# Kernel tuning notes

Hardware: AMD Instinct MI355X
Metric: run time of the kernel (lower is better)

## Reference

```python
import jax, jax.numpy as jnp
import numpy as np
from jax.scipy.special import i0

# NUFFT adjoint (gridding) configuration, matching m_op.plan(uv, (256,256), (512,512), (6,6))
N = 256          # image side
K = 512
J = 6            # kernel support per dim
B = 8            # batch
M = 100000       # n_measurements
ALPHA = K / N    # oversampling = 2
BETA = float(np.pi * np.sqrt((J / ALPHA * (ALPHA - 0.5)) ** 2 - 0.8))  # Fessler KB beta


def setup_inputs() -> dict:
    key = jax.random.key(0)
    k1, k2, k3, k4 = jax.random.split(key, 4)
    y_real = jax.random.normal(k1, (B, M), dtype=jnp.float32)
    y_imag = jax.random.normal(k2, (B, M), dtype=jnp.float32)
    weights = jax.random.uniform(k3, (M,), dtype=jnp.float32, minval=0.1, maxval=1.0)
    uv = jax.random.uniform(k4, (M, 2), dtype=jnp.float32,
                            minval=-np.pi, maxval=np.pi)
    return {"y_real": y_real, "y_imag": y_imag, "weights": weights, "uv": uv}


def _kb(t):
    # Kaiser-Bessel interpolation kernel, support |t| <= J/2
    u = 2.0 * t / J
    return i0(BETA * jnp.sqrt(jnp.clip(1.0 - u * u, 0.0))) / i0(jnp.asarray(BETA, jnp.float32))


def reference(y_real, y_imag, weights, uv):
    # weighted complex measurements: inputs * measurement_weights
    y = (y_real + 1j * y_imag) * weights[None, :]           # (B, M) complex64

    # map uv in [-pi, pi) to oversampled grid coords in [0, K)
    kf = uv * (K / (2.0 * np.pi))                            # (M, 2), DC at index 0 (mod K)
    base = jnp.floor(kf).astype(jnp.int32)                   # (M, 2)
    offs = jnp.arange(-J // 2 + 1, J // 2 + 1)               # [-2..3], 6 taps
    idx = base[:, :, None] + offs[None, None, :]             # (M, 2, J)
    dist = idx.astype(jnp.float32) - kf[:, :, None]
    w = _kb(dist)                                            # (M, 2, J) separable weights
    idxm = jnp.mod(idx, K)                                   # wrap onto torus

    w2 = (w[:, 0, :, None] * w[:, 1, None, :]).reshape(M, J * J)          # (M, 36)
    lin = (idxm[:, 0, :, None] * K + idxm[:, 1, None, :]).reshape(M * J * J)
    vals = (y[:, :, None] * w2[None, :, :].astype(jnp.complex64)).reshape(B, M * J * J)

    # scatter-add onto oversampled Fourier grid
    grid = jnp.zeros((B, K * K), jnp.complex64).at[:, lin].add(vals)
    grid = grid.reshape(B, K, K)

    # inverse FFT, center, crop to N x N
    img = jnp.fft.fftshift(jnp.fft.ifft2(grid), axes=(1, 2))
    c = K // 2
    img = img[:, c - N // 2:c + N // 2, c - N // 2:c + N // 2]

    # deapodization: divide by 1D FT of the KB kernel (always real here since BETA > pi*J/4*... )
    n = jnp.arange(N, dtype=jnp.float32) - N // 2
    xf = np.pi * J * n / K
    arg = BETA * BETA - xf * xf
    d = jnp.sinh(jnp.sqrt(arg)) / jnp.sqrt(arg)              # (N,)
    apod = d[:, None] * d[None, :]

    x = (jnp.real(img) / apod).astype(jnp.float32)           # tf.math.real(adj_op(...))

    # per-image min-max rescale
    tmax = jnp.max(x, axis=(1, 2), keepdims=True)
    tmin = jnp.min(x, axis=(1, 2), keepdims=True)
    return (x - tmin) / (tmax - tmin)
```

## Files before the change

### kernel.cpp

```cpp
#include <hip/hip_runtime.h>
#include <math.h>

#define NN 256
#define KK 512
#define JJ 6
#define BB 8
#define MPTS 100000
#define NBINS (KK * KK)
#define KF_SCALE 81.48733086305615f

typedef _Float16 h8 __attribute__((ext_vector_type(8)));
typedef _Float16 h2 __attribute__((ext_vector_type(2)));


__device__ __forceinline__ float i0f_dev(float x) {
    float ax = fabsf(x);
    if (ax < 3.75f) {
        float t = x / 3.75f; t *= t;
        return 1.0f + t*(3.5156229f + t*(3.0899424f + t*(1.2067492f +
               t*(0.2659732f + t*(0.0360768f + t*0.0045813f)))));
    } else {
        float t = 3.75f / ax;
        return (expf(ax) * rsqrtf(ax)) *
               (0.39894228f + t*(0.01328592f + t*(0.00225319f + t*(-0.00157565f +
                t*(0.00916281f + t*(-0.02057706f + t*(0.02635537f +
                t*(-0.01647633f + t*0.00392377f))))))));
    }
}

__device__ __forceinline__ float kbf(float t, float beta, float inv_i0b) {
    float u = t * (1.0f / 3.0f);
    float q = fmaxf(1.0f - u * u, 0.0f);
    return i0f_dev(beta * sqrtf(q)) * inv_i0b;
}

__device__ __forceinline__ int wave_scan(int x, int lane) {
#pragma unroll
    for (int off = 1; off < 64; off <<= 1) {
        int y = __shfl_up(x, off, 64);
        if (lane >= off) x += y;
    }
    return x;
}

__device__ __forceinline__ void build_row_prefix(const int* __restrict__ btot,
                                                 int* sPref, int t)
{
    if (t < 64) {
        int carry = 0;
        if (t == 0) sPref[0] = 0;
#pragma unroll
        for (int k = 0; k < 8; ++k) {
            int x = btot[k * 64 + t];
            int incl = wave_scan(x, t);
            sPref[k * 64 + t + 1] = incl + carry;
            carry += __shfl(incl, 63, 64);
        }
    }
}

__device__ __forceinline__ float kb_lut(const float* __restrict__ sT, float t) {
    float u = (t + 3.0f) * (1023.0f / 6.0f);
    int i = (int)u;
    i = min(i, 1022);
    float f = u - (float)i;
    float a = sT[i];
    return a + f * (sT[i + 1] - sT[i]);
}

__device__ __forceinline__ void tw_lookup(const float* __restrict__ twc,
                                          const float* __restrict__ tws,
                                          int idx, float& wr, float& wi) {
    float sg = (idx & 256) ? -1.0f : 1.0f;
    int ib = idx & 255;
    wr = sg * twc[ib];
    wi = sg * tws[ib];
}


__device__ __forceinline__ void fill_point(
    const float2* __restrict__ uv2,
    const float* __restrict__ y_real, const float* __restrict__ y_imag,
    const float* __restrict__ weights, const int* __restrict__ offsets,
    const int* sPref,
    int* counts, char* rec, const float* sT, int m)
{
    float2 u = uv2[m];
    float kf0 = u.x * KF_SCALE;
    float kf1 = u.y * KF_SCALE;
    float f0 = floorf(kf0), f1 = floorf(kf1);
    float fr0 = kf0 - f0, fr1 = kf1 - f1;
    int b0r = (int)f0 & (KK - 1);
    int b1c = (int)f1 & (KK - 1);
    int bin = (b0r << 9) | b1c;
    int old = atomicSub(&counts[bin], 1);
    int slot = sPref[b0r] + offsets[bin] + old - 1;

    _Float16 hw[12];
#pragma unroll
    for (int j = 0; j < JJ; ++j) {
        hw[j]     = (_Float16)kb_lut(sT, (float)(j - 2) - fr0);
        hw[6 + j] = (_Float16)kb_lut(sT, (float)(j - 2) - fr1);
    }

    float4 c0v, c1v;
    _Float16* p0 = (_Float16*)&c0v;
    _Float16* p1 = (_Float16*)&c1v;
#pragma unroll
    for (int j = 0; j < 8; ++j) p0[j] = hw[j];
#pragma unroll
    for (int j = 0; j < 4; ++j) p1[j] = hw[8 + j];
    ((int*)&c1v)[2] = b1c;
    ((int*)&c1v)[3] = 0;

    float wm = weights[m];
    h8 ha, hb;
#pragma unroll
    for (int b = 0; b < 4; ++b) {
        ha[2 * b]     = (_Float16)(y_real[b * MPTS + m] * wm);
        ha[2 * b + 1] = (_Float16)(y_imag[b * MPTS + m] * wm);
        hb[2 * b]     = (_Float16)(y_real[(b + 4) * MPTS + m] * wm);
        hb[2 * b + 1] = (_Float16)(y_imag[(b + 4) * MPTS + m] * wm);
    }

    float4* dst = (float4*)(rec + (size_t)slot * 64);
    dst[0] = c0v;
    dst[1] = c1v;
    dst[2] = *(float4*)&ha;
    dst[3] = *(float4*)&hb;
}

__device__ __forceinline__ void gather_strip(
    const int* __restrict__ offsets, const int* sPref,
    const char* __restrict__ rec,
    h2* __restrict__ gridh, char* myl, int j, int w, int lane)
{
    int half = lane >> 5;
    int l32 = lane & 31;
    int xcd = j & 7;
    int c0 = (xcd << 6) + ((j >> 3) & 63);
    int q4 = j >> 9;
    int c1base = (q4 << 7) + (w << 5);
    int c1 = c1base + l32;
    int wa = c1 - 3, wb = c1 + 2;

    float aR[4], aI[4];
#pragma unroll
    for (int b = 0; b < 4; ++b) { aR[b] = 0.0f; aI[b] = 0.0f; }

    for (int j0 = 0; j0 < JJ; ++j0) {
        int r0 = (c0 - (j0 - 2)) & (KK - 1);
        int rowbase = r0 << 9;
        int P = sPref[r0];
        int lo = c1base - 3, hi = c1base + 33;
        int nseg, ga0, gb0, ga1, gb1;
        if (lo < 0)        { ga0 = lo; gb0 = -1;  ga1 = 0;   gb1 = hi; nseg = 2; }
        else if (hi > 511) { ga0 = lo; gb0 = 511; ga1 = 512; gb1 = hi; nseg = 2; }
        else               { ga0 = lo; gb0 = hi;  ga1 = 0;   gb1 = 0;  nseg = 1; }

        for (int sgi = 0; sgi < nseg; ++sgi) {
            int ga = sgi ? ga1 : ga0;
            int gb = sgi ? gb1 : gb0;
            int pstart = P + offsets[rowbase + (ga & 511)];
            int ce = (gb & 511) + 1;
            int pend = (ce == 512) ? sPref[r0 + 1]
                                   : P + offsets[rowbase + ce];
            int ia = max(wa, ga), ib = min(wb, gb);
            bool has = ia <= ib;
            int pA = has ? P + offsets[rowbase + (ia & 511)] : 0;
            int pB = has ? ((ib == gb) ? pend
                                       : P + offsets[rowbase + ((ib + 1) & 511)]) : 0;

            for (int pc = pstart; pc < pend; pc += 32) {
                int cnt = min(32, pend - pc);
                int sub = lane & 3;
                int prow = lane >> 2;
#pragma unroll
                for (int qq = 0; qq < 2; ++qq) {
                    if (16 * qq < cnt) {
                        int pp = min(pc + prow + 16 * qq, MPTS - 1);
                        float4 v = *(const float4*)(rec + (size_t)pp * 64 + sub * 16);
                        *(float4*)(myl + (prow + 16 * qq) * 88 + sub * 16) = v;
                    }
                }
                int pLo = max(pA, pc), pHi = min(pB, pc + cnt);
                for (int p = pLo; p < pHi; ++p) {
                    const char* rp = myl + (p - pc) * 88;
                    int bin1 = *(const int*)(rp + 24);
                    int idx = (c1 - bin1 + 2) & 511;
                    bool ok = idx <= 5;
                    idx = ok ? idx : 0;
                    float w0 = (float)*(const _Float16*)(rp + j0 * 2);
                    float w1 = (float)*(const _Float16*)(rp + 12 + idx * 2);
                    float ww = ok ? w0 * w1 : 0.0f;
                    h8 yv = *(const h8*)(rp + 32 + (half << 4));
#pragma unroll
                    for (int b = 0; b < 4; ++b) {
                        aR[b] += (float)yv[2 * b]     * ww;
                        aI[b] += (float)yv[2 * b + 1] * ww;
                    }
                }
            }
        }
    }

    int c = (c0 << 9) + c1;
#pragma unroll
    for (int b = 0; b < 4; ++b) {
        h2 v;
        v[0] = (_Float16)aR[b];
        v[1] = (_Float16)aI[b];
        gridh[((size_t)((half << 2) + b) << 18) + c] = v;
    }
}

__device__ __forceinline__ void wave_fft512(float xr[8], float xi[8], int lane,
                                            const float* __restrict__ twc,
                                            const float* __restrict__ tws)
{
    float a0r = xr[0]+xr[4], a0i = xi[0]+xi[4];
    float a4r = xr[0]-xr[4], a4i = xi[0]-xi[4];
    float a2r = xr[2]+xr[6], a2i = xi[2]+xi[6];
    float a6r = xr[2]-xr[6], a6i = xi[2]-xi[6];
    float a1r = xr[1]+xr[5], a1i = xi[1]+xi[5];
    float a5r = xr[1]-xr[5], a5i = xi[1]-xi[5];
    float a3r = xr[3]+xr[7], a3i = xi[3]+xi[7];
    float a7r = xr[3]-xr[7], a7i = xi[3]-xi[7];
    float b0r = a0r+a2r, b0i = a0i+a2i;
    float b2r = a0r-a2r, b2i = a0i-a2i;
    float b4r = a4r-a6i, b4i = a4i+a6r;
    float b6r = a4r+a6i, b6i = a4i-a6r;
    float b1r = a1r+a3r, b1i = a1i+a3i;
    float b3r = a1r-a3r, b3i = a1i-a3i;
    float b5r = a5r-a7i, b5i = a5i+a7r;
    float b7r = a5r+a7i, b7i = a5i-a7r;
    const float S2 = 0.70710678118654752f;
    float w5r = S2*(b5r-b5i), w5i = S2*(b5r+b5i);
    float w7r = -S2*(b7r+b7i), w7i = S2*(b7r-b7i);
    float y1r = b4r+w5r, y1i = b4i+w5i;
    float y5r = b4r-w5r, y5i = b4i-w5i;
    float y2r = b2r-b3i, y2i = b2i+b3r;
    float y6r = b2r+b3i, y6i = b2i-b3r;
    float y3r = b6r+w7r, y3i = b6i+w7i;
    float y7r = b6r-w7r, y7i = b6i-w7i;

    int p = __brev((unsigned)lane) >> 26;
    xr[0] = b0r+b1r; xi[0] = b0i+b1i;
    {
        float wr, wi;
        tw_lookup(twc, tws, p,     wr, wi); xr[1] = y1r*wr - y1i*wi; xi[1] = y1i*wr + y1r*wi;
        tw_lookup(twc, tws, p * 2, wr, wi); xr[2] = y2r*wr - y2i*wi; xi[2] = y2i*wr + y2r*wi;
        tw_lookup(twc, tws, p * 3, wr, wi); xr[3] = y3r*wr - y3i*wi; xi[3] = y3i*wr + y3r*wi;
        float y4r = b0r-b1r, y4i = b0i-b1i;
        tw_lookup(twc, tws, p * 4, wr, wi); xr[4] = y4r*wr - y4i*wi; xi[4] = y4i*wr + y4r*wi;
        tw_lookup(twc, tws, p * 5, wr, wi); xr[5] = y5r*wr - y5i*wi; xi[5] = y5i*wr + y5r*wi;
        tw_lookup(twc, tws, p * 6, wr, wi); xr[6] = y6r*wr - y6i*wi; xi[6] = y6i*wr + y6r*wi;
        tw_lookup(twc, tws, p * 7, wr, wi); xr[7] = y7r*wr - y7i*wi; xi[7] = y7i*wr + y7r*wi;
    }

#pragma unroll
    for (int t = 0; t < 6; ++t) {
        int m = 1 << t;
        int j = lane & (m - 1);
        int ti = j << (8 - t);
        float wc = twc[ti], wsn = tws[ti];
        bool hi = (lane & m) != 0;
#pragma unroll
        for (int d = 0; d < 8; ++d) {
            float pR = __shfl_xor(xr[d], m, 64);
            float pI = __shfl_xor(xi[d], m, 64);
            float bR = hi ? xr[d] : pR;
            float bI = hi ? xi[d] : pI;
            float aR = hi ? pR : xr[d];
            float aI = hi ? pI : xi[d];
            float wbR = wc * bR - wsn * bI;
            float wbI = wc * bI + wsn * bR;
            xr[d] = hi ? aR - wbR : aR + wbR;
            xi[d] = hi ? aI - wbI : aI + wbI;
        }
    }
}

__device__ __forceinline__ void wave_fft256(float xr[4], float xi[4], int lane,
                                            const float* __restrict__ twc,
                                            const float* __restrict__ tws)
{
    float t0r = xr[0]+xr[2], t0i = xi[0]+xi[2];
    float t1r = xr[0]-xr[2], t1i = xi[0]-xi[2];
    float t2r = xr[1]+xr[3], t2i = xi[1]+xi[3];
    float t3r = xr[1]-xr[3], t3i = xi[1]-xi[3];
    float y1r = t1r-t3i, y1i = t1i+t3r;
    float y3r = t1r+t3i, y3i = t1i-t3r;

    int p2 = (__brev((unsigned)lane) >> 26) << 1;
    xr[0] = t0r+t2r; xi[0] = t0i+t2i;
    {
        float wr, wi;
        tw_lookup(twc, tws, p2,     wr, wi); xr[1] = y1r*wr - y1i*wi; xi[1] = y1i*wr + y1r*wi;
        float y2r = t0r-t2r, y2i = t0i-t2i;
        tw_lookup(twc, tws, p2 * 2, wr, wi); xr[2] = y2r*wr - y2i*wi; xi[2] = y2i*wr + y2r*wi;
        tw_lookup(twc, tws, p2 * 3, wr, wi); xr[3] = y3r*wr - y3i*wi; xi[3] = y3i*wr + y3r*wi;
    }

#pragma unroll
    for (int t = 0; t < 6; ++t) {
        int m = 1 << t;
        int j = lane & (m - 1);
        int ti = j << (8 - t);
        float wc = twc[ti], wsn = tws[ti];
        bool hi = (lane & m) != 0;
#pragma unroll
        for (int d = 0; d < 4; ++d) {
            float pR = __shfl_xor(xr[d], m, 64);
            float pI = __shfl_xor(xi[d], m, 64);
            float bR = hi ? xr[d] : pR;
            float bI = hi ? xi[d] : pI;
            float aR = hi ? pR : xr[d];
            float aI = hi ? pI : xi[d];
            float wbR = wc * bR - wsn * bI;
            float wbI = wc * bI + wsn * bR;
            xr[d] = hi ? aR - wbR : aR + wbR;
            xi[d] = hi ? aI - wbI : aI + wbI;
        }
    }
}

__device__ __forceinline__ void fftA_body(const h2* __restrict__ gridh,
                                          h2* __restrict__ Ch, int bx, int t,
                                          float* sR, float* sI,
                                          float* twc, float* tws)
{
    int lane = t & 63;
    int w = t >> 6;
    int x  = bx & 7;
    int b  = (bx >> 3) & 7;
    int k1base = (x << 6) | (((bx >> 6) & 7) << 3);
    int k1 = k1base + w;

    if (t < 256) {
        float ang = (float)(2.0 * M_PI / 512.0) * (float)t;
        float s, c; sincosf(ang, &s, &c);
        twc[t] = c; tws[t] = s;
    }

    const h2* row = gridh + ((size_t)b << 18) + ((size_t)k1 << 9);
    int p = __brev((unsigned)lane) >> 26;
    float xr[8], xi[8];
#pragma unroll
    for (int a = 0; a < 8; ++a) {
        h2 v = row[p + (a << 6)];
        xr[a] = (float)v[0]; xi[a] = (float)v[1];
    }
    __syncthreads();

    wave_fft512(xr, xi, lane, twc, tws);

    bool act = (lane < 16) | (lane >= 48);
    int lpp = (lane < 16) ? lane : (lane - 32);
    if (act) {
#pragma unroll
        for (int d = 0; d < 8; ++d) {
            int addr = w * 264 + d * 33 + lpp;
            sR[addr] = xr[d];
            sI[addr] = xi[d];
        }
    }
    __syncthreads();

#pragma unroll
    for (int pp = 0; pp < 4; ++pp) {
        int idx = pp * 512 + t;
        int kk = idx & 7;
        int s2 = idx >> 3;
        int v = (s2 + 128) & 255;
        int d = v & 7;
        int lp = v >> 3;
        int addr = kk * 264 + d * 33 + lp;
        h2 o;
        o[0] = (_Float16)sR[addr];
        o[1] = (_Float16)sI[addr];
        Ch[(((size_t)(b << 8) + s2) << 9) + k1base + kk] = o;
    }
}

__device__ __forceinline__ void fftB_body(const h2* __restrict__ Ch,
                                          float* __restrict__ imgT, float beta2,
                                          float* __restrict__ pmin,
                                          float* __restrict__ pmax,
                                          int bx, int t,
                                          float* twc, float* tws, float* invd,
                                          float (*wor)[256], float* wmn, float* wmx)
{
    int lane = t & 63;
    int w = t >> 6;
    int row = w >> 1;
    int odd = w & 1;
    int rowid = bx * 4 + row;
    int b = rowid >> 8;
    int s2 = rowid & 255;

    if (t < 256) {
        float ang = (float)(2.0 * M_PI / 512.0) * (float)t;
        float s, c; sincosf(ang, &s, &c);
        twc[t] = c; tws[t] = s;
    } else if (t < 512) {
        int i = t - 256;
        const float XF = (float)(M_PI * (double)JJ / (double)KK);
        float n = (float)(i - 128);
        float xf = XF * n;
        float arg = beta2 - xf * xf;
        float sq = sqrtf(arg);
        invd[i] = sq / sinhf(sq);
    }

    const h2* rowp = Ch + ((size_t)rowid << 9);
    int p = __brev((unsigned)lane) >> 26;
    float xr[4], xi[4];
#pragma unroll
    for (int a = 0; a < 4; ++a) {
        h2 v = rowp[((p + (a << 6)) << 1) | odd];
        xr[a] = (float)v[0]; xi[a] = (float)v[1];
    }
    __syncthreads();

    wave_fft256(xr, xi, lane, twc, tws);

    if (odd) {
        float4 wo;
#pragma unroll
        for (int d = 0; d < 4; ++d) {
            int k = (lane << 2) + d;
            ((float*)&wo)[d] = xr[d] * twc[k] - xi[d] * tws[k];
        }
        *(float4*)&wor[row][lane << 2] = wo;
    }
    __syncthreads();

    if (!odd) {
        const float INVK2 = 1.0f / ((float)KK * (float)KK);
        float sbase = INVK2 * invd[s2];
        float lmin = 1e30f, lmax = -1e30f;
        float4 wo = *(const float4*)&wor[row][lane << 2];
        float vals[4];
#pragma unroll
        for (int d = 0; d < 4; ++d) {
            int k = (lane << 2) + d;
            float e = xr[d];
            float woK = ((const float*)&wo)[d];
            float xre = (k < 128) ? (e + woK) : (e - woK);
            int r = (k + 128) & 255;
            float o = xre * sbase * invd[r];
            vals[d] = o;
            lmin = fminf(lmin, o);
            lmax = fmaxf(lmax, o);
        }
        int r0run = ((lane << 2) + 128) & 255;
        *(float4*)(imgT + ((size_t)b << 16) + (s2 << 8) + r0run) =
            make_float4(vals[0], vals[1], vals[2], vals[3]);
#pragma unroll
        for (int off = 32; off >= 1; off >>= 1) {
            lmin = fminf(lmin, __shfl_xor(lmin, off, 64));
            lmax = fmaxf(lmax, __shfl_xor(lmax, off, 64));
        }
        if (lane == 0) { wmn[row] = lmin; wmx[row] = lmax; }
    }
    __syncthreads();
    if (t == 0) {
        float mn = fminf(fminf(wmn[0], wmn[1]), fminf(wmn[2], wmn[3]));
        float mx = fmaxf(fmaxf(wmx[0], wmx[1]), fmaxf(wmx[2], wmx[3]));
        pmin[bx] = mn;
        pmax[bx] = mx;
    }
}

__device__ __forceinline__ void norm_body(const float* __restrict__ imgT,
                                          const float* __restrict__ pmin,
                                          const float* __restrict__ pmax,
                                          float* __restrict__ out,
                                          int bx, int t, int nthr,
                                          float (*tile)[65], float* s_mn, float* s_inv)
{
    int b = bx >> 4;
    int tl = bx & 15;
    int r0 = (tl & 3) << 6;
    int s0 = (tl >> 2) << 6;
    int tr = t & 63;
    int ts = t >> 6;
    int nts = nthr >> 6;

    if (t < 64) {
        float mn = pmin[(b << 6) + t];
        float mx = pmax[(b << 6) + t];
#pragma unroll
        for (int off = 32; off >= 1; off >>= 1) {
            mn = fminf(mn, __shfl_xor(mn, off, 64));
            mx = fmaxf(mx, __shfl_xor(mx, off, 64));
        }
        if (t == 0) { *s_mn = mn; *s_inv = 1.0f / (mx - mn); }
    }

    const float* src = imgT + ((size_t)b << 16);
    for (int s2i = ts; s2i < 64; s2i += nts)
        tile[s2i][tr] = src[((s0 + s2i) << 8) + r0 + tr];
    __syncthreads();

    float mn = *s_mn, inv = *s_inv;
    float* dst = out + ((size_t)b << 16);
    for (int ri = ts; ri < 64; ri += nts)
        dst[((r0 + ri) << 8) + s0 + tr] = (tile[tr][ri] - mn) * inv;
}


__global__ __launch_bounds__(256) void count_bins(
    const float2* __restrict__ uv2, int* __restrict__ counts,
    float* __restrict__ lut, float beta, float inv_i0b)
{
    int m = blockIdx.x * 256 + threadIdx.x;
    if (m < 1024) {
        float t = -3.0f + (6.0f / 1023.0f) * (float)m;
        lut[m] = kbf(t, beta, inv_i0b);
    }
    if (m >= MPTS) return;
    float2 u = uv2[m];
    int b0 = (int)floorf(u.x * KF_SCALE) & (KK - 1);
    int b1 = (int)floorf(u.y * KF_SCALE) & (KK - 1);
    atomicAdd(&counts[(b0 << 9) | b1], 1);
}

__global__ __launch_bounds__(512) void scan_a(
    const int* __restrict__ counts, int* __restrict__ offsets,
    int* __restrict__ btot)
{
    __shared__ int part[8];
    int t = threadIdx.x;
    int lane = t & 63;
    int w8 = t >> 6;
    int gid = blockIdx.x * 512 + t;

    int v = counts[gid];
    int x = wave_scan(v, lane);
    if (lane == 63) part[w8] = x;
    __syncthreads();
    if (t < 8) {
        int pq = part[t];
#pragma unroll
        for (int off = 1; off < 8; off <<= 1) {
            int y = __shfl_up(pq, off, 64);
            if (t >= off) pq += y;
        }
        part[t] = pq;
    }
    __syncthreads();
    int incl = x + ((w8 > 0) ? part[w8 - 1] : 0);
    offsets[gid] = incl - v;
    if (t == 511) btot[blockIdx.x] = incl;
}

__global__ __launch_bounds__(256) void fill_records(
    const float2* __restrict__ uv2,
    const float* __restrict__ y_real, const float* __restrict__ y_imag,
    const float* __restrict__ weights, const int* __restrict__ offsets,
    const int* __restrict__ btot,
    int* __restrict__ counts, char* __restrict__ rec,
    const float* __restrict__ lut)
{
    __shared__ float sT[1024];
    __shared__ int sPref[513];
    int tid = threadIdx.x;
#pragma unroll
    for (int q = 0; q < 4; ++q) sT[q * 256 + tid] = lut[q * 256 + tid];
    build_row_prefix(btot, sPref, tid);
    __syncthreads();
    int m = blockIdx.x * 256 + tid;
    if (m >= MPTS) return;
    fill_point(uv2, y_real, y_imag, weights, offsets, sPref, counts, rec, sT, m);
}

__global__ __launch_bounds__(256) void gather_grid(
    const int* __restrict__ offsets, const int* __restrict__ btot,
    const char* __restrict__ rec, h2* __restrict__ gridh)
{
    __shared__ __align__(16) char lds[4][2816];
    __shared__ int sPref[513];
    int t = threadIdx.x;
    build_row_prefix(btot, sPref, t);
    __syncthreads();
    gather_strip(offsets, sPref, rec, gridh, lds[t >> 6], blockIdx.x,
                 t >> 6, t & 63);
}

__global__ __launch_bounds__(512) void fftA(
    const h2* __restrict__ gridh, h2* __restrict__ Ch)
{
    __shared__ float sR[2112], sI[2112];
    __shared__ float twc[256], tws[256];
    fftA_body(gridh, Ch, blockIdx.x, threadIdx.x, sR, sI, twc, tws);
}

__global__ __launch_bounds__(512) void fftB(
    const h2* __restrict__ Ch, float* __restrict__ imgT, float beta2,
    float* __restrict__ pmin, float* __restrict__ pmax)
{
    __shared__ float twc[256], tws[256];
    __shared__ float invd[256];
    __shared__ __align__(16) float wor[4][256];
    __shared__ float wmn[4], wmx[4];
    fftB_body(Ch, imgT, beta2, pmin, pmax, blockIdx.x, threadIdx.x,
              twc, tws, invd, wor, wmn, wmx);
}

__global__ __launch_bounds__(256) void norm_t(
    const float* __restrict__ imgT, const float* __restrict__ pmin,
    const float* __restrict__ pmax, float* __restrict__ out)
{
    __shared__ float tile[64][65];
    __shared__ float s_mn, s_inv;
    norm_body(imgT, pmin, pmax, out, blockIdx.x, threadIdx.x, 256,
              tile, &s_mn, &s_inv);
}


static double i0_host(double x) {
    double sum = 1.0, term = 1.0;
    double q = x * x * 0.25;
    for (int k = 1; k < 80; ++k) {
        term *= q / ((double)k * (double)k);
        sum += term;
        if (term < sum * 1e-17) break;
    }
    return sum;
}

extern "C" void kernel_launch(void* const* d_in, const int* in_sizes, int n_in,
                              void* d_out, int out_size, void* d_ws, size_t ws_size,
                              hipStream_t stream)
{
    const float* y_real  = (const float*)d_in[0];
    const float* y_imag  = (const float*)d_in[1];
    const float* weights = (const float*)d_in[2];
    const float2* uv2    = (const float2*)d_in[3];
    float* out = (float*)d_out;

    char* W = (char*)d_ws;
    h2*       gridh   = (h2*)W;
    int*      counts  = (int*)W;
    float*    imgT    = (float*)W;
    char*     A       = W + (size_t)16 * 1024 * 1024;
    char*     rec     = A;
    int*      offsets = (int*)(A + 6400000);
    h2*       Ch      = (h2*)A;
    float*    pmin    = (float*)(A + 8400000);
    float*    pmax    = (float*)(A + 8402048);
    float*    lut     = (float*)(A + 8404096);
    int*      btot    = (int*)(A + 8408192);

    double beta_d = M_PI * sqrt(19.45);
    float beta = (float)beta_d;
    float inv_i0b = (float)(1.0 / i0_host(beta_d));
    float beta2 = (float)(beta_d * beta_d);

    hipMemsetAsync(counts, 0, NBINS * sizeof(int), stream);

    count_bins<<<(MPTS + 255) / 256, 256, 0, stream>>>(
        uv2, counts, lut, beta, inv_i0b);

    scan_a<<<512, 512, 0, stream>>>(counts, offsets, btot);

    fill_records<<<(MPTS + 255) / 256, 256, 0, stream>>>(
        uv2, y_real, y_imag, weights, offsets, btot, counts, rec, lut);

    gather_grid<<<2048, 256, 0, stream>>>(offsets, btot, rec, gridh);

    fftA<<<512, 512, 0, stream>>>(gridh, Ch);

    fftB<<<512, 512, 0, stream>>>(Ch, imgT, beta2, pmin, pmax);

    norm_t<<<128, 256, 0, stream>>>(imgT, pmin, pmax, out);
}
```

Before: 139.2 us.

## Gather per-lane bin ranges directly from global records, dropping the LDS staging

The gather kernel used to stage each strip's point records into LDS cooperatively in chunks of 32, and every lane scanned the whole window while masking out bins it did not own. Now each lane loads the bin offsets once, shares them across the wave with shuffles, and walks only the points in its own six neighbouring column bins, reading records straight from global memory. This removes the LDS copy traffic and the wasted masked iterations. In exchange, lanes run divergent loop trip counts and make scattered global loads that depend on the cache to absorb neighbouring lanes re-reading the same records.

```diff
diff --git a/kernel.cpp b/kernel.cpp
--- a/kernel.cpp
+++ b/kernel.cpp
@@ -133,7 +133,7 @@
 __device__ __forceinline__ void gather_strip(
     const int* __restrict__ offsets, const int* sPref,
     const char* __restrict__ rec,
-    h2* __restrict__ gridh, char* myl, int j, int w, int lane)
+    h2* __restrict__ gridh, int j, int w, int lane)
 {
     int half = lane >> 5;
     int l32 = lane & 31;
@@ -142,7 +142,6 @@
     int q4 = j >> 9;
     int c1base = (q4 << 7) + (w << 5);
     int c1 = c1base + l32;
-    int wa = c1 - 3, wb = c1 + 2;
 
     float aR[4], aI[4];
 #pragma unroll
@@ -152,55 +151,30 @@
         int r0 = (c0 - (j0 - 2)) & (KK - 1);
         int rowbase = r0 << 9;
         int P = sPref[r0];
-        int lo = c1base - 3, hi = c1base + 33;
-        int nseg, ga0, gb0, ga1, gb1;
-        if (lo < 0)        { ga0 = lo; gb0 = -1;  ga1 = 0;   gb1 = hi; nseg = 2; }
-        else if (hi > 511) { ga0 = lo; gb0 = 511; ga1 = 512; gb1 = hi; nseg = 2; }
-        else               { ga0 = lo; gb0 = hi;  ga1 = 0;   gb1 = 0;  nseg = 1; }
-
-        for (int sgi = 0; sgi < nseg; ++sgi) {
-            int ga = sgi ? ga1 : ga0;
-            int gb = sgi ? gb1 : gb0;
-            int pstart = P + offsets[rowbase + (ga & 511)];
-            int ce = (gb & 511) + 1;
-            int pend = (ce == 512) ? sPref[r0 + 1]
-                                   : P + offsets[rowbase + ce];
-            int ia = max(wa, ga), ib = min(wb, gb);
-            bool has = ia <= ib;
-            int pA = has ? P + offsets[rowbase + (ia & 511)] : 0;
-            int pB = has ? ((ib == gb) ? pend
-                                       : P + offsets[rowbase + ((ib + 1) & 511)]) : 0;
-
-            for (int pc = pstart; pc < pend; pc += 32) {
-                int cnt = min(32, pend - pc);
-                int sub = lane & 3;
-                int prow = lane >> 2;
-#pragma unroll
-                for (int qq = 0; qq < 2; ++qq) {
-                    if (16 * qq < cnt) {
-                        int pp = min(pc + prow + 16 * qq, MPTS - 1);
-                        float4 v = *(const float4*)(rec + (size_t)pp * 64 + sub * 16);
-                        *(float4*)(myl + (prow + 16 * qq) * 88 + sub * 16) = v;
-                    }
-                }
-                int pLo = max(pA, pc), pHi = min(pB, pc + cnt);
-                for (int p = pLo; p < pHi; ++p) {
-                    const char* rp = myl + (p - pc) * 88;
-                    int bin1 = *(const int*)(rp + 24);
-                    int idx = (c1 - bin1 + 2) & 511;
-                    bool ok = idx <= 5;
-                    idx = ok ? idx : 0;
-                    float w0 = (float)*(const _Float16*)(rp + j0 * 2);
-                    float w1 = (float)*(const _Float16*)(rp + 12 + idx * 2);
-                    float ww = ok ? w0 * w1 : 0.0f;
-                    h8 yv = *(const h8*)(rp + 32 + (half << 4));
-#pragma unroll
-                    for (int b = 0; b < 4; ++b) {
-                        aR[b] += (float)yv[2 * b]     * ww;
-                        aI[b] += (float)yv[2 * b + 1] * ww;
-                    }
+        int rowEnd = sPref[r0 + 1];
+
+        int li = min(lane, 37);
+        int vec = offsets[rowbase + ((c1base - 3 + li) & 511)];
+
+        int ps = P + __shfl(vec, l32, 64);
+#pragma unroll
+        for (int d = 0; d < 6; ++d) {
+            int b1 = (c1 - 3 + d) & 511;
+            int nxt = P + __shfl(vec, l32 + d + 1, 64);
+            int pe = (b1 == 511) ? rowEnd : nxt;
+            for (int p = ps; p < pe; ++p) {
+                const char* rp = rec + (size_t)p * 64;
+                float w0 = (float)*(const _Float16*)(rp + j0 * 2);
+                float w1 = (float)*(const _Float16*)(rp + 12 + (5 - d) * 2);
+                float ww = w0 * w1;
+                h8 yv = *(const h8*)(rp + 32 + (half << 4));
+#pragma unroll
+                for (int b = 0; b < 4; ++b) {
+                    aR[b] += (float)yv[2 * b]     * ww;
+                    aI[b] += (float)yv[2 * b + 1] * ww;
                 }
             }
+            ps = nxt;
         }
     }
 
@@ -580,13 +554,11 @@
     const int* __restrict__ offsets, const int* __restrict__ btot,
     const char* __restrict__ rec, h2* __restrict__ gridh)
 {
-    __shared__ __align__(16) char lds[4][2816];
     __shared__ int sPref[513];
     int t = threadIdx.x;
     build_row_prefix(btot, sPref, t);
     __syncthreads();
-    gather_strip(offsets, sPref, rec, gridh, lds[t >> 6], blockIdx.x,
-                 t >> 6, t & 63);
+    gather_strip(offsets, sPref, rec, gridh, blockIdx.x, t >> 6, t & 63);
 }
 
 __global__ __launch_bounds__(512) void fftA(
```

Result: slower. 155.6 us (+11.8%).

## Prefetch next row's records and batch offset lookups in gather fast path

Applied to the files above, without the earlier changes.

Adds a non-wrapping fast path to the gather kernel. It loads all six rows' offset vectors up front in one lane-parallel read and takes the per-lane boundaries with shuffles. The first chunk of point records for the next row is software-prefetched into registers while the current row is being accumulated, to hide global-load latency. Strips that wrap around the grid edge still use the old path, and the extra prefetch registers may reduce occupancy.

```diff
diff --git a/kernel.cpp b/kernel.cpp
--- a/kernel.cpp
+++ b/kernel.cpp
@@ -130,7 +130,29 @@
     dst[3] = *(float4*)&hb;
 }
 
-__device__ __forceinline__ void gather_strip(
+__device__ __forceinline__ void gather_accum(
+    const char* myl, int pLo, int pHi, int pc, int c1, int j0, int half,
+    float aR[4], float aI[4])
+{
+    for (int p = pLo; p < pHi; ++p) {
+        const char* rp = myl + (p - pc) * 88;
+        int bin1 = *(const int*)(rp + 24);
+        int idx = (c1 - bin1 + 2) & 511;
+        bool ok = idx <= 5;
+        idx = ok ? idx : 0;
+        float w0 = (float)*(const _Float16*)(rp + j0 * 2);
+        float w1 = (float)*(const _Float16*)(rp + 12 + idx * 2);
+        float ww = ok ? w0 * w1 : 0.0f;
+        h8 yv = *(const h8*)(rp + 32 + (half << 4));
+#pragma unroll
+        for (int b = 0; b < 4; ++b) {
+            aR[b] += (float)yv[2 * b]     * ww;
+            aI[b] += (float)yv[2 * b + 1] * ww;
+        }
+    }
+}
+
+__device__ void gather_strip_wrap(
     const int* __restrict__ offsets, const int* sPref,
     const char* __restrict__ rec,
     h2* __restrict__ gridh, char* myl, int j, int w, int lane)
@@ -152,6 +174,7 @@
         int r0 = (c0 - (j0 - 2)) & (KK - 1);
         int rowbase = r0 << 9;
         int P = sPref[r0];
+        int rowEnd = sPref[r0 + 1];
         int lo = c1base - 3, hi = c1base + 33;
         int nseg, ga0, gb0, ga1, gb1;
         if (lo < 0)        { ga0 = lo; gb0 = -1;  ga1 = 0;   gb1 = hi; nseg = 2; }
@@ -163,8 +186,7 @@
             int gb = sgi ? gb1 : gb0;
             int pstart = P + offsets[rowbase + (ga & 511)];
             int ce = (gb & 511) + 1;
-            int pend = (ce == 512) ? sPref[r0 + 1]
-                                   : P + offsets[rowbase + ce];
+            int pend = (ce == 512) ? rowEnd : P + offsets[rowbase + ce];
             int ia = max(wa, ga), ib = min(wb, gb);
             bool has = ia <= ib;
             int pA = has ? P + offsets[rowbase + (ia & 511)] : 0;
@@ -183,23 +205,8 @@
                         *(float4*)(myl + (prow + 16 * qq) * 88 + sub * 16) = v;
                     }
                 }
-                int pLo = max(pA, pc), pHi = min(pB, pc + cnt);
-                for (int p = pLo; p < pHi; ++p) {
-                    const char* rp = myl + (p - pc) * 88;
-                    int bin1 = *(const int*)(rp + 24);
-                    int idx = (c1 - bin1 + 2) & 511;
-                    bool ok = idx <= 5;
-                    idx = ok ? idx : 0;
-                    float w0 = (float)*(const _Float16*)(rp + j0 * 2);
-                    float w1 = (float)*(const _Float16*)(rp + 12 + idx * 2);
-                    float ww = ok ? w0 * w1 : 0.0f;
-                    h8 yv = *(const h8*)(rp + 32 + (half << 4));
-#pragma unroll
-                    for (int b = 0; b < 4; ++b) {
-                        aR[b] += (float)yv[2 * b]     * ww;
-                        aI[b] += (float)yv[2 * b + 1] * ww;
-                    }
-                }
+                gather_accum(myl, max(pA, pc), min(pB, pc + cnt), pc,
+                             c1, j0, half, aR, aI);
             }
         }
     }
@@ -585,8 +592,97 @@
     int t = threadIdx.x;
     build_row_prefix(btot, sPref, t);
     __syncthreads();
-    gather_strip(offsets, sPref, rec, gridh, lds[t >> 6], blockIdx.x,
-                 t >> 6, t & 63);
+
+    int w = t >> 6;
+    int lane = t & 63;
+    int j = blockIdx.x;
+    int half = lane >> 5;
+    int l32 = lane & 31;
+    int xcd = j & 7;
+    int c0 = (xcd << 6) + ((j >> 3) & 63);
+    int q4 = j >> 9;
+    int c1base = (q4 << 7) + (w << 5);
+    int c1 = c1base + l32;
+    char* myl = lds[w];
+
+    if (c1base == 0 || c1base + 33 > 511) {
+        gather_strip_wrap(offsets, sPref, rec, gridh, myl, j, w, lane);
+        return;
+    }
+
+    int lo = c1base - 3;
+    int li = min(lane, 37);
+    int sub = lane & 3;
+    int prow = lane >> 2;
+
+    float aR[4], aI[4];
+#pragma unroll
+    for (int b = 0; b < 4; ++b) { aR[b] = 0.0f; aI[b] = 0.0f; }
+
+    int vec[6], Pj[6];
+#pragma unroll
+    for (int j0 = 0; j0 < 6; ++j0) {
+        int r0 = (c0 - (j0 - 2)) & (KK - 1);
+        Pj[j0] = sPref[r0];
+        vec[j0] = offsets[(r0 << 9) + lo + li];
+    }
+
+    int ps_cur = Pj[0] + __shfl(vec[0], 0, 64);
+    float4 pend0, pend1;
+    {
+        int pp0 = min(ps_cur + prow, MPTS - 1);
+        int pp1 = min(ps_cur + prow + 16, MPTS - 1);
+        pend0 = *(const float4*)(rec + (size_t)pp0 * 64 + sub * 16);
+        pend1 = *(const float4*)(rec + (size_t)pp1 * 64 + sub * 16);
+    }
+
+#pragma unroll
+    for (int j0 = 0; j0 < 6; ++j0) {
+        int ps = ps_cur;
+        int pe = Pj[j0] + __shfl(vec[j0], 37, 64);
+        int pA = Pj[j0] + __shfl(vec[j0], l32, 64);
+        int pB = Pj[j0] + __shfl(vec[j0], l32 + 6, 64);
+        int cnt = min(32, pe - ps);
+
+        if (0 < cnt)
+            *(float4*)(myl + prow * 88 + sub * 16) = pend0;
+        if (16 < cnt)
+            *(float4*)(myl + (prow + 16) * 88 + sub * 16) = pend1;
+
+        if (j0 < 5) {
+            ps_cur = Pj[j0 + 1] + __shfl(vec[j0 + 1], 0, 64);
+            int pp0 = min(ps_cur + prow, MPTS - 1);
+            int pp1 = min(ps_cur + prow + 16, MPTS - 1);
+            pend0 = *(const float4*)(rec + (size_t)pp0 * 64 + sub * 16);
+            pend1 = *(const float4*)(rec + (size_t)pp1 * 64 + sub * 16);
+        }
+
+        gather_accum(myl, max(pA, ps), min(pB, ps + cnt), ps,
+                     c1, j0, half, aR, aI);
+
+        for (int pc = ps + 32; pc < pe; pc += 32) {
+            int cnt2 = min(32, pe - pc);
+#pragma unroll
+            for (int qq = 0; qq < 2; ++qq) {
+                if (16 * qq < cnt2) {
+                    int pp = min(pc + prow + 16 * qq, MPTS - 1);
+                    float4 v = *(const float4*)(rec + (size_t)pp * 64 + sub * 16);
+                    *(float4*)(myl + (prow + 16 * qq) * 88 + sub * 16) = v;
+                }
+            }
+            gather_accum(myl, max(pA, pc), min(pB, pc + cnt2), pc,
+                         c1, j0, half, aR, aI);
+        }
+    }
+
+    int c = (c0 << 9) + c1;
+#pragma unroll
+    for (int b = 0; b < 4; ++b) {
+        h2 v;
+        v[0] = (_Float16)aR[b];
+        v[1] = (_Float16)aI[b];
+        gridh[((size_t)((half << 2) + b) << 18) + c] = v;
+    }
 }
 
 __global__ __launch_bounds__(512) void fftA(
```

After: 139.8 us. No clear change (+0.4%).
